# Kernel tuning notes

Measured on AMD Instinct MI355X. Metric: run time of the kernel, lower is better.

Reference implementation:

```python
import jax, jax.numpy as jnp
import numpy as np

B, C, H, W = 8, 64, 64, 64  # module requires c == h == w due to view/permute quirk


def setup_inputs() -> dict:
    key = jax.random.key(0)
    ks = jax.random.split(key, 5)
    return {
        "x": jax.random.normal(ks[0], (B, C, H, W), dtype=jnp.float32),
        "w_qkv": jax.random.normal(ks[1], (3 * C, C), dtype=jnp.float32) * (1.0 / np.sqrt(C)),
        "b_qkv": jax.random.normal(ks[2], (3 * C,), dtype=jnp.float32) * 0.02,
        "w_out": jax.random.normal(ks[3], (C, C), dtype=jnp.float32) * (1.0 / np.sqrt(C)),
        "b_out": jax.random.normal(ks[4], (C,), dtype=jnp.float32) * 0.02,
    }


def reference(x, w_qkv, b_qkv, w_out, b_out):
    b, c, h, w = x.shape
    # 1x1 conv == channel matmul (norm='none' -> Identity, the only runnable branch)
    qkv = jnp.einsum('bchw,oc->bohw', x, w_qkv) + b_qkv[None, :, None, None]
    q, k, v = jnp.split(qkv, 3, axis=1)  # each (b, c, h, w)

    def flat(t):  # (b,c,h,w) -> (b, h*w, c), matches permute(0,2,3,1).view
        return t.transpose(0, 2, 3, 1).reshape(b, h * w, c)

    q, k, v = flat(q), flat(k), flat(v)
    scale = 1.0 / jnp.sqrt(jnp.asarray(c, dtype=x.dtype))
    scores = jax.nn.softmax(jnp.einsum('bqc,bkc->bqk', q, k) * scale, axis=-1)
    out = jnp.einsum('bqk,bkc->bqc', scores, v)  # (b, hw, c)
    # Faithfully replicate the original's view(b,c,h,w).permute(0,3,1,2) quirk
    out = out.reshape(b, c, h, w).transpose(0, 3, 1, 2)  # (b, w, c, h); needs c==h==w
    out = jnp.einsum('bchw,oc->bohw', out, w_out) + b_out[None, :, None, None]
    return out + x
```

## Files before the change

kernel.cpp:

```cpp
#include <hip/hip_runtime.h>
#include <hip/hip_bf16.h>
#include <stdint.h>

typedef unsigned short u16;
typedef __attribute__((ext_vector_type(8))) short bf16x8;
typedef __attribute__((ext_vector_type(4))) float f32x4;
typedef __attribute__((ext_vector_type(2))) float f32x2;
typedef __attribute__((ext_vector_type(4))) unsigned int u32x4;
typedef __attribute__((ext_vector_type(2))) unsigned int u32x2;

#define NTOK 4096
#define NT32 32

#if __has_builtin(__builtin_amdgcn_exp2f)
#define EXP2F __builtin_amdgcn_exp2f
#else
#define EXP2F exp2f
#endif

__device__ __forceinline__ f32x4 MFMA(bf16x8 a, bf16x8 b, f32x4 c) {
    return __builtin_amdgcn_mfma_f32_16x16x32_bf16(a, b, c, 0, 0, 0);
}

__device__ __forceinline__ uint32_t pk_bf16(float a, float b) {
    uint32_t d;
    asm("v_cvt_pk_bf16_f32 %0, %1, %2" : "=v"(d) : "v"(a), "v"(b));
    return d;
}

__device__ __forceinline__ void hilo_pack8(const float* v, bf16x8* h, bf16x8* l) {
    union { uint32_t u[4]; bf16x8 b; } H, L;
#pragma unroll
    for (int m = 0; m < 4; ++m) {
        const uint32_t ua = __float_as_uint(v[2*m]);
        const uint32_t ub = __float_as_uint(v[2*m+1]);
        const float la = v[2*m]   - __uint_as_float(ua & 0xffff0000u);
        const float lb = v[2*m+1] - __uint_as_float(ub & 0xffff0000u);
        H.u[m] = (ua >> 16) | (ub & 0xffff0000u);
        L.u[m] = (__float_as_uint(la) >> 16) | (__float_as_uint(lb) & 0xffff0000u);
    }
    *h = H.b; *l = L.b;
}

__global__ __launch_bounds__(256) void k_qkv(
    const float* __restrict__ x, const float* __restrict__ wqkv, const float* __restrict__ bqkv,
    u16* __restrict__ Qp, u16* __restrict__ Kp, u16* __restrict__ Vp)
{
    __shared__ float qt_lds[64 * 194];
    const int blk = blockIdx.x;
    const int b   = blk >> 6;
    const int tb  = (blk & 63) << 6;
    const int tid = threadIdx.x;
    const int lane = tid & 63;
    const int wv  = __builtin_amdgcn_readfirstlane(tid >> 6);
    const int r   = lane & 15;
    const int g   = lane >> 4;
    const int o0  = wv * 48;

    bf16x8 wh[3][2], wl[3][2];
#pragma unroll
    for (int oi = 0; oi < 3; ++oi)
#pragma unroll
        for (int ks = 0; ks < 2; ++ks) {
            const float* wp = wqkv + (size_t)(o0 + oi*16 + r) * 64 + ks*32 + g*8;
            float wv8[8];
            *(f32x4*)(wv8)     = *(const f32x4*)(wp);
            *(f32x4*)(wv8 + 4) = *(const f32x4*)(wp + 4);
            hilo_pack8(wv8, &wh[oi][ks], &wl[oi][ks]);
        }

    f32x4 acc[3][4];
#pragma unroll
    for (int oi = 0; oi < 3; ++oi)
#pragma unroll
        for (int tt = 0; tt < 4; ++tt) acc[oi][tt] = 0.f;

#pragma unroll
    for (int tt = 0; tt < 4; ++tt) {
        bf16x8 xh[2], xl[2];
#pragma unroll
        for (int ks = 0; ks < 2; ++ks) {
            float xv[8];
#pragma unroll
            for (int j = 0; j < 8; ++j)
                xv[j] = x[(size_t)(b*64 + ks*32 + g*8 + j) * NTOK + tb + tt*16 + r];
            hilo_pack8(xv, &xh[ks], &xl[ks]);
        }
#pragma unroll
        for (int oi = 0; oi < 3; ++oi) {
            f32x4 a = acc[oi][tt];
            a = MFMA(wh[oi][0], xh[0], a);
            a = MFMA(wh[oi][1], xh[1], a);
            a = MFMA(wl[oi][0], xh[0], a);
            a = MFMA(wl[oi][1], xh[1], a);
            a = MFMA(wh[oi][0], xl[0], a);
            a = MFMA(wh[oi][1], xl[1], a);
            acc[oi][tt] = a;
        }
    }

#pragma unroll
    for (int oi = 0; oi < 3; ++oi)
#pragma unroll
        for (int tt = 0; tt < 4; ++tt)
#pragma unroll
            for (int i = 0; i < 4; ++i)
                qt_lds[(tt*16 + r) * 194 + o0 + oi*16 + g*4 + i] = acc[oi][tt][i];
    __syncthreads();

    const float SC = 0.18033688011112042f;

    {
        const int t = tid >> 2, c0 = (tid & 3) * 16;
        float v[16], bq[16];
#pragma unroll
        for (int m = 0; m < 8; ++m)
            *(f32x2*)(v + 2*m) = *(const f32x2*)&qt_lds[t*194 + c0 + 2*m];
#pragma unroll
        for (int m = 0; m < 4; ++m)
            *(f32x4*)(bq + 4*m) = *(const f32x4*)(bqkv + c0 + 4*m);
        u32x4 P0, P1;
#pragma unroll
        for (int m = 0; m < 4; ++m) {
            P0[m] = pk_bf16((v[2*m]   + bq[2*m]  ) * SC, (v[2*m+1] + bq[2*m+1]) * SC);
            P1[m] = pk_bf16((v[8+2*m] + bq[8+2*m]) * SC, (v[9+2*m] + bq[9+2*m]) * SC);
        }
        size_t base = ((size_t)(b * NTOK + tb + t)) * 64 + c0;
        *(u32x4*)(Qp + base)     = P0;
        *(u32x4*)(Qp + base + 8) = P1;
    }

#pragma unroll
    for (int uu = 0; uu < 2; ++uu) {
        const int u  = tid * 2 + uu;
        const int t  = u >> 3;
        const int ks = (u >> 2) & 1;
        const int gk = u & 3;
        const int cb0 = 64 + ks*32 + gk*8;
        float v[8];
#pragma unroll
        for (int m = 0; m < 4; ++m)
            *(f32x2*)(v + 2*m) = *(const f32x2*)&qt_lds[t*194 + cb0 + 2*m];
        u32x4 P;
#pragma unroll
        for (int m = 0; m < 4; ++m)
            P[m] = pk_bf16(v[2*m] + bqkv[cb0 + 2*m], v[2*m+1] + bqkv[cb0 + 2*m+1]);
        const int tg = tb + t;
        size_t kbase = (size_t)b * 262144 + ((size_t)(tg >> 4) * 2 + ks) * 512 + gk*128 + (t & 15) * 8;
        *(u32x4*)(Kp + kbase) = P;
    }

    {
        const int cb = (tid >> 4) & 3;
        const int r2 = tid & 15;
        const float bv = bqkv[128 + cb*16 + r2];
        const int T = (blk & 63) >> 1;
        const int halfb = blk & 1;
#pragma unroll
        for (int m = 0; m < 4; ++m) {
            const int tq = m * 4 + (tid >> 6);
            float v[4];
#pragma unroll
            for (int jj = 0; jj < 4; ++jj)
                v[jj] = qt_lds[(tq*4 + jj)*194 + 128 + cb*16 + r2] + bv;
            const int t = tq * 4;
            const int wtr = halfb*2 + (t >> 5);
            const int sti = (t >> 4) & 1;
            const int g2  = (t >> 2) & 3;
            u32x2 W;
            W[0] = pk_bf16(v[0], v[1]);
            W[1] = pk_bf16(v[2], v[3]);
            size_t vbase = (size_t)b * 262144 +
                           (((size_t)T * 4 + wtr) * 4 + cb) * 512 + (g2*16 + r2) * 8 + sti * 4;
            *(u32x2*)(Vp + vbase) = W;
        }
    }
}

__global__ __launch_bounds__(256, 2) void k_attn(
    const u16* __restrict__ Qp, const u16* __restrict__ Kp, const u16* __restrict__ Vp,
    const float* __restrict__ wout, const float* __restrict__ bout,
    const float* __restrict__ x, float* __restrict__ out)
{
    __shared__ float marr[4][4][16];
    __shared__ float larr[4][4][16];
    __shared__ float otbuf[2][64 * 67];
    const int hw  = blockIdx.x;
    const int b   = hw & 7;
    const int qt  = hw >> 3;
    const int tid = threadIdx.x;
    const int lane = tid & 63;
    const int wt  = tid >> 6;
    const int r   = lane & 15;
    const int g   = lane >> 4;

    bf16x8 qh[4][2];
#pragma unroll
    for (int rt = 0; rt < 4; ++rt) {
        const int t1 = qt * 64 + rt * 16 + r;
        const size_t qoff = ((size_t)(b * NTOK + t1)) * 64 + g * 8;
        qh[rt][0] = *(const bf16x8*)(Qp + qoff);
        qh[rt][1] = *(const bf16x8*)(Qp + qoff + 32);
    }

    const u16* Kb = Kp + (size_t)b * 262144;
    const u16* Vb = Vp + (size_t)b * 262144;

    f32x4 oacc[4][4];
#pragma unroll
    for (int rt = 0; rt < 4; ++rt)
#pragma unroll
        for (int cb = 0; cb < 4; ++cb) oacc[rt][cb] = 0.f;
    float mrun[4] = {-1e30f, -1e30f, -1e30f, -1e30f};
    float lpart[4] = {0.f, 0.f, 0.f, 0.f};

    bf16x8 kc[2][2];
#pragma unroll
    for (int sti = 0; sti < 2; ++sti)
#pragma unroll
        for (int ks = 0; ks < 2; ++ks)
            kc[sti][ks] = *(const bf16x8*)(Kb + ((((size_t)0 + wt*2 + sti) * 2 + ks) * 64 + lane) * 8);

    for (int T = 0; T < NT32; ++T) {
        bf16x8 vf[4];
#pragma unroll
        for (int cb = 0; cb < 4; ++cb)
            vf[cb] = *(const bf16x8*)(Vb + ((((size_t)T * 4 + wt) * 4 + cb) * 64 + lane) * 8);

        const int Tn = (T + 1 < NT32) ? T + 1 : T;
        bf16x8 kn[2][2];
#pragma unroll
        for (int sti = 0; sti < 2; ++sti)
#pragma unroll
            for (int ks = 0; ks < 2; ++ks)
                kn[sti][ks] = *(const bf16x8*)(Kb + ((((size_t)Tn * 8 + wt*2 + sti) * 2 + ks) * 64 + lane) * 8);

        f32x4 s[4][2];
#pragma unroll
        for (int rt = 0; rt < 4; ++rt)
#pragma unroll
            for (int sti = 0; sti < 2; ++sti) {
                f32x4 a = 0.f;
                a = MFMA(kc[sti][0], qh[rt][0], a);
                a = MFMA(kc[sti][1], qh[rt][1], a);
                s[rt][sti] = a;
            }

        float m8[4];
#pragma unroll
        for (int rt = 0; rt < 4; ++rt) {
            float a = fmaxf(fmaxf(s[rt][0][0], s[rt][0][1]), fmaxf(s[rt][0][2], s[rt][0][3]));
            float c = fmaxf(fmaxf(s[rt][1][0], s[rt][1][1]), fmaxf(s[rt][1][2], s[rt][1][3]));
            m8[rt] = fmaxf(a, c);
        }
        const bool need = (m8[0] > mrun[0] + 8.f) || (m8[1] > mrun[1] + 8.f) ||
                          (m8[2] > mrun[2] + 8.f) || (m8[3] > mrun[3] + 8.f);
        if (__any(need)) {
#pragma unroll
            for (int rt = 0; rt < 4; ++rt) {
                float mr = fmaxf(m8[rt], __shfl_xor(m8[rt], 16));
                mr = fmaxf(mr, __shfl_xor(mr, 32));
                const float mnew = fmaxf(mrun[rt], mr);
                const float corr = EXP2F(mrun[rt] - mnew);
                lpart[rt] *= corr;
                float c4[4];
#pragma unroll
                for (int i = 0; i < 4; ++i) c4[i] = __shfl(corr, g * 4 + i);
#pragma unroll
                for (int cb = 0; cb < 4; ++cb)
#pragma unroll
                    for (int i = 0; i < 4; ++i) oacc[rt][cb][i] *= c4[i];
                mrun[rt] = mnew;
            }
        }

#pragma unroll
        for (int rt = 0; rt < 4; ++rt) {
            float p[8];
            float ls = 0.f;
#pragma unroll
            for (int sti = 0; sti < 2; ++sti)
#pragma unroll
                for (int i = 0; i < 4; ++i) {
                    const float pv = EXP2F(s[rt][sti][i] - mrun[rt]);
                    p[sti*4 + i] = pv; ls += pv;
                }
            lpart[rt] += ls;
            union { uint32_t u[4]; bf16x8 b; } PA;
#pragma unroll
            for (int m = 0; m < 4; ++m) PA.u[m] = pk_bf16(p[2*m], p[2*m+1]);
#pragma unroll
            for (int cb = 0; cb < 4; ++cb)
                oacc[rt][cb] = MFMA(PA.b, vf[cb], oacc[rt][cb]);
        }

#pragma unroll
        for (int sti = 0; sti < 2; ++sti)
#pragma unroll
            for (int ks = 0; ks < 2; ++ks)
                kc[sti][ks] = kn[sti][ks];
    }

    float lsum[4];
#pragma unroll
    for (int rt = 0; rt < 4; ++rt) {
        float v = lpart[rt];
        v += __shfl_xor(v, 16);
        v += __shfl_xor(v, 32);
        lsum[rt] = v;
    }
    if (lane < 16) {
#pragma unroll
        for (int rt = 0; rt < 4; ++rt) {
            marr[wt][rt][lane] = mrun[rt];
            larr[wt][rt][lane] = lsum[rt];
        }
    }
    __syncthreads();

    float w4[4][4];
#pragma unroll
    for (int rt = 0; rt < 4; ++rt) {
        const float m0 = marr[0][rt][r], m1 = marr[1][rt][r];
        const float m2 = marr[2][rt][r], m3 = marr[3][rt][r];
        const float mstar = fmaxf(fmaxf(m0, m1), fmaxf(m2, m3));
        const float lstar = larr[0][rt][r] * EXP2F(m0 - mstar)
                          + larr[1][rt][r] * EXP2F(m1 - mstar)
                          + larr[2][rt][r] * EXP2F(m2 - mstar)
                          + larr[3][rt][r] * EXP2F(m3 - mstar);
        const float wsc = EXP2F(mrun[rt] - mstar) / lstar;
#pragma unroll
        for (int i = 0; i < 4; ++i) w4[rt][i] = __shfl(wsc, g * 4 + i);
    }

    if (wt < 2) {
        float* ob = otbuf[wt];
#pragma unroll
        for (int rt = 0; rt < 4; ++rt)
#pragma unroll
            for (int cb = 0; cb < 4; ++cb)
#pragma unroll
                for (int i = 0; i < 4; ++i)
                    ob[(rt*16 + g*4 + i)*67 + cb*16 + r] = oacc[rt][cb][i] * w4[rt][i];
    }
    __syncthreads();
    if (wt >= 2) {
        float* ob = otbuf[wt - 2];
#pragma unroll
        for (int rt = 0; rt < 4; ++rt)
#pragma unroll
            for (int cb = 0; cb < 4; ++cb)
#pragma unroll
                for (int i = 0; i < 4; ++i)
                    ob[(rt*16 + g*4 + i)*67 + cb*16 + r] += oacc[rt][cb][i] * w4[rt][i];
    }
    __syncthreads();

    bf16x8 oh[2], ol[2];
#pragma unroll
    for (int ks = 0; ks < 2; ++ks) {
        float ov[8];
#pragma unroll
        for (int j = 0; j < 8; ++j) {
            const int idx = (wt*16 + r)*67 + ks*32 + g*8 + j;
            ov[j] = otbuf[0][idx] + otbuf[1][idx];
        }
        hilo_pack8(ov, &oh[ks], &ol[ks]);
    }
    f32x4 acc2[4];
#pragma unroll
    for (int ot = 0; ot < 4; ++ot) {
        bf16x8 wh2[2], wl2[2];
#pragma unroll
        for (int ks = 0; ks < 2; ++ks) {
            const float* wp = wout + (size_t)(ot*16 + r) * 64 + ks*32 + g*8;
            float wv8[8];
            *(f32x4*)(wv8)     = *(const f32x4*)(wp);
            *(f32x4*)(wv8 + 4) = *(const f32x4*)(wp + 4);
            hilo_pack8(wv8, &wh2[ks], &wl2[ks]);
        }
        f32x4 a = 0.f;
        a = MFMA(wh2[0], oh[0], a);
        a = MFMA(wh2[1], oh[1], a);
        a = MFMA(wl2[0], oh[0], a);
        a = MFMA(wl2[1], oh[1], a);
        a = MFMA(wh2[0], ol[0], a);
        a = MFMA(wh2[1], ol[1], a);
        acc2[ot] = a;
    }
#pragma unroll
    for (int ot = 0; ot < 4; ++ot)
#pragma unroll
        for (int i = 0; i < 4; ++i) {
            const int oo = ot*16 + g*4 + i;
            const size_t xi = ((size_t)(b*64 + oo)) * NTOK + qt*64 + wt*16 + r;
            out[xi] = acc2[ot][i] + bout[oo] + x[xi];
        }
}

extern "C" void kernel_launch(void* const* d_in, const int* in_sizes, int n_in,
                              void* d_out, int out_size, void* d_ws, size_t ws_size,
                              hipStream_t stream)
{
    (void)in_sizes; (void)n_in; (void)out_size; (void)ws_size;
    const float* x    = (const float*)d_in[0];
    const float* wqkv = (const float*)d_in[1];
    const float* bqkv = (const float*)d_in[2];
    const float* wout = (const float*)d_in[3];
    const float* bout = (const float*)d_in[4];
    float* out = (float*)d_out;

    char* ws = (char*)d_ws;
    const size_t MB = 1024 * 1024;
    u16* Qp = (u16*)(ws);
    u16* Kp = (u16*)(ws + 4 * MB);
    u16* Vp = (u16*)(ws + 8 * MB);

    k_qkv<<<512, 256, 0, stream>>>(x, wqkv, bqkv, Qp, Kp, Vp);
    k_attn<<<512, 256, 0, stream>>>(Qp, Kp, Vp, wout, bout, x, out);
}
```

Baseline: 63.20 us.

## Split attention block across 8 waves with double-buffered K and MFMA priority

Doubles the attention block to 512 threads, so each wave handles 32 query rows instead of 64 while keeping the 4-way key split. K fragments are double-buffered across two iterations in place of a copy per iteration, and s_setprio raises priority around the MFMA sections. The goal is more waves in flight and lower register pressure to hide global-load latency. The cost is that each wave now loads every K/V fragment for half as many queries, which doubles K/V traffic per block, and the output projection is split across more waves.

```diff
diff --git a/kernel.cpp b/kernel.cpp
--- a/kernel.cpp
+++ b/kernel.cpp
@@ -177,27 +177,29 @@
     }
 }
 
-__global__ __launch_bounds__(256, 2) void k_attn(
+__global__ __launch_bounds__(512, 4) void k_attn(
     const u16* __restrict__ Qp, const u16* __restrict__ Kp, const u16* __restrict__ Vp,
     const float* __restrict__ wout, const float* __restrict__ bout,
     const float* __restrict__ x, float* __restrict__ out)
 {
-    __shared__ float marr[4][4][16];
-    __shared__ float larr[4][4][16];
+    __shared__ float marr[8][2][16];
+    __shared__ float larr[8][2][16];
     __shared__ float otbuf[2][64 * 67];
     const int hw  = blockIdx.x;
     const int b   = hw & 7;
     const int qt  = hw >> 3;
     const int tid = threadIdx.x;
     const int lane = tid & 63;
-    const int wt  = tid >> 6;
+    const int wv  = tid >> 6;
+    const int wq  = wv >> 2;
+    const int wt2 = wv & 3;
     const int r   = lane & 15;
     const int g   = lane >> 4;
 
-    bf16x8 qh[4][2];
-#pragma unroll
-    for (int rt = 0; rt < 4; ++rt) {
-        const int t1 = qt * 64 + rt * 16 + r;
+    bf16x8 qh[2][2];
+#pragma unroll
+    for (int rt = 0; rt < 2; ++rt) {
+        const int t1 = qt * 64 + wq * 32 + rt * 16 + r;
         const size_t qoff = ((size_t)(b * NTOK + t1)) * 64 + g * 8;
         qh[rt][0] = *(const bf16x8*)(Qp + qoff);
         qh[rt][1] = *(const bf16x8*)(Qp + qoff + 32);
@@ -206,58 +208,61 @@
     const u16* Kb = Kp + (size_t)b * 262144;
     const u16* Vb = Vp + (size_t)b * 262144;
 
-    f32x4 oacc[4][4];
-#pragma unroll
-    for (int rt = 0; rt < 4; ++rt)
+    f32x4 oacc[2][4];
+#pragma unroll
+    for (int rt = 0; rt < 2; ++rt)
 #pragma unroll
         for (int cb = 0; cb < 4; ++cb) oacc[rt][cb] = 0.f;
-    float mrun[4] = {-1e30f, -1e30f, -1e30f, -1e30f};
-    float lpart[4] = {0.f, 0.f, 0.f, 0.f};
-
-    bf16x8 kc[2][2];
+    float mrun[2] = {-1e30f, -1e30f};
+    float lpart[2] = {0.f, 0.f};
+
+    bf16x8 kA[2][2], kB[2][2];
 #pragma unroll
     for (int sti = 0; sti < 2; ++sti)
 #pragma unroll
-        for (int ks = 0; ks < 2; ++ks)
-            kc[sti][ks] = *(const bf16x8*)(Kb + ((((size_t)0 + wt*2 + sti) * 2 + ks) * 64 + lane) * 8);
-
-    for (int T = 0; T < NT32; ++T) {
+        for (int ks = 0; ks < 2; ++ks) {
+            kA[sti][ks] = *(const bf16x8*)(Kb + ((((size_t)0*8 + wt2*2 + sti) * 2 + ks) * 64 + lane) * 8);
+            kB[sti][ks] = *(const bf16x8*)(Kb + ((((size_t)1*8 + wt2*2 + sti) * 2 + ks) * 64 + lane) * 8);
+        }
+
+    auto body = [&](bf16x8 (&kb)[2][2], int T, int Tp) {
         bf16x8 vf[4];
 #pragma unroll
         for (int cb = 0; cb < 4; ++cb)
-            vf[cb] = *(const bf16x8*)(Vb + ((((size_t)T * 4 + wt) * 4 + cb) * 64 + lane) * 8);
-
-        const int Tn = (T + 1 < NT32) ? T + 1 : T;
-        bf16x8 kn[2][2];
-#pragma unroll
-        for (int sti = 0; sti < 2; ++sti)
-#pragma unroll
-            for (int ks = 0; ks < 2; ++ks)
-                kn[sti][ks] = *(const bf16x8*)(Kb + ((((size_t)Tn * 8 + wt*2 + sti) * 2 + ks) * 64 + lane) * 8);
-
-        f32x4 s[4][2];
-#pragma unroll
-        for (int rt = 0; rt < 4; ++rt)
+            vf[cb] = *(const bf16x8*)(Vb + ((((size_t)T * 4 + wt2) * 4 + cb) * 64 + lane) * 8);
+
+        f32x4 s[2][2];
+        __builtin_amdgcn_s_setprio(1);
+#pragma unroll
+        for (int rt = 0; rt < 2; ++rt)
 #pragma unroll
             for (int sti = 0; sti < 2; ++sti) {
                 f32x4 a = 0.f;
-                a = MFMA(kc[sti][0], qh[rt][0], a);
-                a = MFMA(kc[sti][1], qh[rt][1], a);
+                a = MFMA(kb[sti][0], qh[rt][0], a);
+                a = MFMA(kb[sti][1], qh[rt][1], a);
                 s[rt][sti] = a;
             }
-
-        float m8[4];
-#pragma unroll
-        for (int rt = 0; rt < 4; ++rt) {
+        __builtin_amdgcn_s_setprio(0);
+
+        if (Tp < NT32) {
+#pragma unroll
+            for (int sti = 0; sti < 2; ++sti)
+#pragma unroll
+                for (int ks = 0; ks < 2; ++ks)
+                    kb[sti][ks] = *(const bf16x8*)(Kb + ((((size_t)Tp*8 + wt2*2 + sti) * 2 + ks) * 64 + lane) * 8);
+        }
+
+        float m8[2];
+#pragma unroll
+        for (int rt = 0; rt < 2; ++rt) {
             float a = fmaxf(fmaxf(s[rt][0][0], s[rt][0][1]), fmaxf(s[rt][0][2], s[rt][0][3]));
             float c = fmaxf(fmaxf(s[rt][1][0], s[rt][1][1]), fmaxf(s[rt][1][2], s[rt][1][3]));
             m8[rt] = fmaxf(a, c);
         }
-        const bool need = (m8[0] > mrun[0] + 8.f) || (m8[1] > mrun[1] + 8.f) ||
-                          (m8[2] > mrun[2] + 8.f) || (m8[3] > mrun[3] + 8.f);
+        const bool need = (m8[0] > mrun[0] + 8.f) || (m8[1] > mrun[1] + 8.f);
         if (__any(need)) {
 #pragma unroll
-            for (int rt = 0; rt < 4; ++rt) {
+            for (int rt = 0; rt < 2; ++rt) {
                 float mr = fmaxf(m8[rt], __shfl_xor(m8[rt], 16));
                 mr = fmaxf(mr, __shfl_xor(mr, 32));
                 const float mnew = fmaxf(mrun[rt], mr);
@@ -275,7 +280,7 @@
         }
 
 #pragma unroll
-        for (int rt = 0; rt < 4; ++rt) {
+        for (int rt = 0; rt < 2; ++rt) {
             float p[8];
             float ls = 0.f;
 #pragma unroll
@@ -289,21 +294,22 @@
             union { uint32_t u[4]; bf16x8 b; } PA;
 #pragma unroll
             for (int m = 0; m < 4; ++m) PA.u[m] = pk_bf16(p[2*m], p[2*m+1]);
+            __builtin_amdgcn_s_setprio(1);
 #pragma unroll
             for (int cb = 0; cb < 4; ++cb)
                 oacc[rt][cb] = MFMA(PA.b, vf[cb], oacc[rt][cb]);
-        }
-
-#pragma unroll
-        for (int sti = 0; sti < 2; ++sti)
-#pragma unroll
-            for (int ks = 0; ks < 2; ++ks)
-                kc[sti][ks] = kn[sti][ks];
-    }
-
-    float lsum[4];
-#pragma unroll
-    for (int rt = 0; rt < 4; ++rt) {
+            __builtin_amdgcn_s_setprio(0);
+        }
+    };
+
+    for (int T = 0; T < NT32; T += 2) {
+        body(kA, T,     T + 2);
+        body(kB, T + 1, T + 3);
+    }
+
+    float lsum[2];
+#pragma unroll
+    for (int rt = 0; rt < 2; ++rt) {
         float v = lpart[rt];
         v += __shfl_xor(v, 16);
         v += __shfl_xor(v, 32);
@@ -311,89 +317,91 @@
     }
     if (lane < 16) {
 #pragma unroll
-        for (int rt = 0; rt < 4; ++rt) {
-            marr[wt][rt][lane] = mrun[rt];
-            larr[wt][rt][lane] = lsum[rt];
+        for (int rt = 0; rt < 2; ++rt) {
+            marr[wv][rt][lane] = mrun[rt];
+            larr[wv][rt][lane] = lsum[rt];
         }
     }
     __syncthreads();
 
-    float w4[4][4];
-#pragma unroll
-    for (int rt = 0; rt < 4; ++rt) {
-        const float m0 = marr[0][rt][r], m1 = marr[1][rt][r];
-        const float m2 = marr[2][rt][r], m3 = marr[3][rt][r];
+    float w4[2][4];
+#pragma unroll
+    for (int rt = 0; rt < 2; ++rt) {
+        const float m0 = marr[wq*4+0][rt][r], m1 = marr[wq*4+1][rt][r];
+        const float m2 = marr[wq*4+2][rt][r], m3 = marr[wq*4+3][rt][r];
         const float mstar = fmaxf(fmaxf(m0, m1), fmaxf(m2, m3));
-        const float lstar = larr[0][rt][r] * EXP2F(m0 - mstar)
-                          + larr[1][rt][r] * EXP2F(m1 - mstar)
-                          + larr[2][rt][r] * EXP2F(m2 - mstar)
-                          + larr[3][rt][r] * EXP2F(m3 - mstar);
+        const float lstar = larr[wq*4+0][rt][r] * EXP2F(m0 - mstar)
+                          + larr[wq*4+1][rt][r] * EXP2F(m1 - mstar)
+                          + larr[wq*4+2][rt][r] * EXP2F(m2 - mstar)
+                          + larr[wq*4+3][rt][r] * EXP2F(m3 - mstar);
         const float wsc = EXP2F(mrun[rt] - mstar) / lstar;
 #pragma unroll
         for (int i = 0; i < 4; ++i) w4[rt][i] = __shfl(wsc, g * 4 + i);
     }
 
-    if (wt < 2) {
-        float* ob = otbuf[wt];
-#pragma unroll
-        for (int rt = 0; rt < 4; ++rt)
+    if (wt2 < 2) {
+        float* ob = otbuf[wt2];
+#pragma unroll
+        for (int rt = 0; rt < 2; ++rt)
 #pragma unroll
             for (int cb = 0; cb < 4; ++cb)
 #pragma unroll
                 for (int i = 0; i < 4; ++i)
-                    ob[(rt*16 + g*4 + i)*67 + cb*16 + r] = oacc[rt][cb][i] * w4[rt][i];
+                    ob[(wq*32 + rt*16 + g*4 + i)*67 + cb*16 + r] = oacc[rt][cb][i] * w4[rt][i];
     }
     __syncthreads();
-    if (wt >= 2) {
-        float* ob = otbuf[wt - 2];
-#pragma unroll
-        for (int rt = 0; rt < 4; ++rt)
+    if (wt2 >= 2) {
+        float* ob = otbuf[wt2 - 2];
+#pragma unroll
+        for (int rt = 0; rt < 2; ++rt)
 #pragma unroll
             for (int cb = 0; cb < 4; ++cb)
 #pragma unroll
                 for (int i = 0; i < 4; ++i)
-                    ob[(rt*16 + g*4 + i)*67 + cb*16 + r] += oacc[rt][cb][i] * w4[rt][i];
+                    ob[(wq*32 + rt*16 + g*4 + i)*67 + cb*16 + r] += oacc[rt][cb][i] * w4[rt][i];
     }
     __syncthreads();
 
-    bf16x8 oh[2], ol[2];
+    const int tg = wv & 3;
+    const int oh = wv >> 2;
+    bf16x8 oh_[2], ol_[2];
 #pragma unroll
     for (int ks = 0; ks < 2; ++ks) {
         float ov[8];
 #pragma unroll
         for (int j = 0; j < 8; ++j) {
-            const int idx = (wt*16 + r)*67 + ks*32 + g*8 + j;
+            const int idx = (tg*16 + r)*67 + ks*32 + g*8 + j;
             ov[j] = otbuf[0][idx] + otbuf[1][idx];
         }
-        hilo_pack8(ov, &oh[ks], &ol[ks]);
-    }
-    f32x4 acc2[4];
-#pragma unroll
-    for (int ot = 0; ot < 4; ++ot) {
+        hilo_pack8(ov, &oh_[ks], &ol_[ks]);
+    }
+    f32x4 acc2[2];
+#pragma unroll
+    for (int ot = 0; ot < 2; ++ot) {
         bf16x8 wh2[2], wl2[2];
 #pragma unroll
         for (int ks = 0; ks < 2; ++ks) {
-            const float* wp = wout + (size_t)(ot*16 + r) * 64 + ks*32 + g*8;
+            const float* wp = wout + (size_t)((oh*2 + ot)*16 + r) * 64 + ks*32 + g*8;
             float wv8[8];
             *(f32x4*)(wv8)     = *(const f32x4*)(wp);
             *(f32x4*)(wv8 + 4) = *(const f32x4*)(wp + 4);
             hilo_pack8(wv8, &wh2[ks], &wl2[ks]);
         }
         f32x4 a = 0.f;
-        a = MFMA(wh2[0], oh[0], a);
-        a = MFMA(wh2[1], oh[1], a);
-        a = MFMA(wl2[0], oh[0], a);
-        a = MFMA(wl2[1], oh[1], a);
-        a = MFMA(wh2[0], ol[0], a);
-        a = MFMA(wh2[1], ol[1], a);
+        a = MFMA(wh2[0], oh_[0], a);
+        a = MFMA(wh2[1], oh_[1], a);
+        a = MFMA(wl2[0], oh_[0], a);
+        a = MFMA(wl2[1], oh_[1], a);
+        a = MFMA(wh2[0], ol_[0], a);
+        a = MFMA(wh2[1], ol_[1], a);
         acc2[ot] = a;
     }
 #pragma unroll
-    for (int ot = 0; ot < 4; ++ot)
+    for (int ot = 0; ot < 2; ++ot)
 #pragma unroll
         for (int i = 0; i < 4; ++i) {
-            const int oo = ot*16 + g*4 + i;
-            const size_t xi = ((size_t)(b*64 + oo)) * NTOK + qt*64 + wt*16 + r;
+            const int oo = (oh*2 + ot)*16 + g*4 + i;
+            const size_t xi = ((size_t)(b*64 + oo)) * NTOK + qt*64 + tg*16 + r;
             out[xi] = acc2[ot][i] + bout[oo] + x[xi];
         }
 }
@@ -417,5 +425,5 @@
     u16* Vp = (u16*)(ws + 8 * MB);
 
     k_qkv<<<512, 256, 0, stream>>>(x, wqkv, bqkv, Qp, Kp, Vp);
-    k_attn<<<512, 256, 0, stream>>>(Qp, Kp, Vp, wout, bout, x, out);
-}
+    k_attn<<<512, 512, 0, stream>>>(Qp, Kp, Vp, wout, bout, x, out);
+}
```

New measurement: 166.8 us. +163.9%, slower.
